# Kernel optimization log

Measured on AMD Instinct MI355X. Metric: run time of the kernel, lower is better.

## Reference

```python
import jax, jax.numpy as jnp
import numpy as np
from jax import lax

B, IN_N, MID_N, OUT_N, K, L, WH = 16, 256, 256, 256, 3, 4096, 1024
EPS = 1e-5


def att_conv(x, W, b=None):
    # x: [B, Cin, L], W: [B, Cout, Cin, K] -> per-sample conv1d, padding='same'
    pl, pr = (K - 1) // 2, K // 2
    xp = jnp.pad(x, ((0, 0), (0, 0), (pl, pr)))
    out = 0.
    for t in range(K):  # small fixed K, unrolled shifted-slice einsum
        out = out + jnp.einsum('bcl,boc->bol', lax.dynamic_slice_in_dim(xp, t, L, 2), W[..., t])
    if b is not None:
        out = out + b[:, :, None]
    return out


def batch_norm(x, w, b):
    # training-mode BN over (N, L) per channel, biased variance
    mean = x.mean((0, 2), keepdims=True)
    var = ((x - mean) ** 2).mean((0, 2), keepdims=True)
    return (x - mean) * (w[None, :, None] / jnp.sqrt(var + EPS)) + b[None, :, None]


def se_module(x, w1, b1, w2, b2):
    s = x.mean(2, keepdims=True)  # [B, C, 1]
    s = jax.nn.relu(jnp.einsum('bcl,oc->bol', s, w1) + b1[None, :, None])
    s = jax.nn.sigmoid(jnp.einsum('bcl,oc->bol', s, w2) + b2[None, :, None])
    return x * s


def setup_inputs() -> dict:
    key = jax.random.key(0)
    ks = jax.random.split(key, 16)
    f = lambda k, sh, sc=0.02: jax.random.normal(k, sh, jnp.float32) * sc
    return {
        'x': f(ks[0], (B, IN_N, L), 1.0),
        'att1': f(ks[1], (B, MID_N, WH), 1.0),
        'att2': f(ks[2], (B, MID_N, WH), 1.0),
        'att3': f(ks[3], (B, OUT_N, WH), 1.0),
        'w1_w': f(ks[4], (IN_N * K, WH)), 'w1_b': jnp.zeros((IN_N * K,), jnp.float32),
        'w2_w': f(ks[5], (MID_N * K, WH)), 'w2_b': jnp.zeros((MID_N * K,), jnp.float32),
        'w3_w': f(ks[6], (MID_N * K, WH)), 'w3_b': jnp.zeros((MID_N * K,), jnp.float32),
        'b1_w': f(ks[7], (1, WH)), 'b1_b': jnp.zeros((1,), jnp.float32),
        'bn2_w': jnp.full((MID_N,), 0.1, jnp.float32), 'bn2_b': jnp.zeros((MID_N,), jnp.float32),
        'bn3_w': jnp.full((OUT_N,), 0.1, jnp.float32), 'bn3_b': jnp.zeros((OUT_N,), jnp.float32),
        'se1_w': f(ks[8], (OUT_N, OUT_N)), 'se1_b': jnp.zeros((OUT_N,), jnp.float32),
        'se2_w': f(ks[9], (OUT_N, OUT_N)), 'se2_b': jnp.zeros((OUT_N,), jnp.float32),
    }


def reference(x, att1, att2, att3, w1_w, w1_b, w2_w, w2_b, w3_w, w3_b,
              b1_w, b1_b, bn2_w, bn2_b, bn3_w, bn3_b, se1_w, se1_b, se2_w, se2_b):
    shortcut = x  # in_n == out_n, no downsample -> Identity
    # hypernetwork weight generation (Linear on last dim)
    W1 = (att1 @ w1_w.T + w1_b).reshape(B, MID_N, IN_N, K)
    W2 = (att2 @ w2_w.T + w2_b).reshape(B, MID_N, MID_N, K)
    W3 = (att3 @ w3_w.T + w3_b).reshape(B, OUT_N, MID_N, K)
    b1 = (att1 @ b1_w.T + b1_b)[..., 0]  # [B, mid_n]
    h = jax.nn.relu(att_conv(x, W1, b1))
    h = jax.nn.relu(batch_norm(att_conv(h, W2), bn2_w, bn2_b))
    h = jax.nn.relu(batch_norm(att_conv(h, W3), bn3_w, bn3_b))
    out = jax.nn.relu(se_module(h, se1_w, se1_b, se2_w, se2_b) + shortcut)
    return out
```

## Files before the change

### kernel.cpp

```cpp
#include <hip/hip_runtime.h>
#include <hip/hip_bf16.h>

using bf16 = __hip_bfloat16;
typedef __attribute__((ext_vector_type(4))) float f32x4;
typedef __attribute__((ext_vector_type(8))) short short8;
typedef __attribute__((ext_vector_type(2))) unsigned int uint2v;
typedef __attribute__((ext_vector_type(4))) unsigned int uint4v;

#define DEVI static __device__ __forceinline__

DEVI unsigned short f2b(float f){
  unsigned int u = __float_as_uint(f);
  unsigned int r = (u + 0x7fffu + ((u >> 16) & 1u)) >> 16;
  return (unsigned short)r;
}
DEVI float b2f(unsigned short u){
  return __uint_as_float(((unsigned int)u) << 16);
}

DEVI void gload16(const void* g, void* l){
  __builtin_amdgcn_global_load_lds(
      (const __attribute__((address_space(1))) unsigned int*)g,
      (__attribute__((address_space(3))) unsigned int*)l, 16, 0, 0);
}

__global__ __launch_bounds__(256) void k_transpose_x(const float* __restrict__ x,
                                                     bf16* __restrict__ xt)
{
  __shared__ float tile[64][65];
  const int b = blockIdx.z, l0 = blockIdx.x*64, c0 = blockIdx.y*64;
  const int tid = threadIdx.x;
  {
    const int r = tid >> 2, q = tid & 3;
    const float* src = x + ((size_t)(b*256 + c0 + r))*4096 + l0 + q*16;
    #pragma unroll
    for (int j = 0; j < 4; ++j){
      const f32x4 v = *reinterpret_cast<const f32x4*>(src + j*4);
      #pragma unroll
      for (int e = 0; e < 4; ++e) tile[r][q*16 + j*4 + e] = v[e];
    }
  }
  __syncthreads();
  {
    const int jr = tid >> 2, cq = tid & 3;
    unsigned int w[8];
    #pragma unroll
    for (int e = 0; e < 8; ++e){
      const float lo = tile[cq*16 + 2*e][jr];
      const float hi = tile[cq*16 + 2*e + 1][jr];
      w[e] = (unsigned int)f2b(lo) | ((unsigned int)f2b(hi) << 16);
    }
    unsigned short* dst = (unsigned short*)xt + ((size_t)b*4098 + l0 + jr + 1)*256 + c0 + cq*16;
    uint4v a0 = {w[0],w[1],w[2],w[3]}, a1 = {w[4],w[5],w[6],w[7]};
    *reinterpret_cast<uint4v*>(dst)     = a0;
    *reinterpret_cast<uint4v*>(dst + 8) = a1;
  }
}

__global__ void k_zero_pads(bf16* __restrict__ xt, bf16* __restrict__ h1t)
{
  const int b = blockIdx.x, tid = threadIdx.x;
  const size_t top = (size_t)b*4098*256 + tid;
  const size_t bot = (size_t)b*4098*256 + (size_t)4097*256 + tid;
  unsigned short* px = (unsigned short*)xt;
  unsigned short* ph = (unsigned short*)h1t;
  px[top] = 0; px[bot] = 0; ph[top] = 0; ph[bot] = 0;
}

__global__ __launch_bounds__(256) void k_cvt3(const float* __restrict__ s0, const float* __restrict__ s1,
                                              const float* __restrict__ s2, bf16* __restrict__ dst, int n1)
{
  const size_t total = (size_t)3 * (size_t)n1 / 4;
  for (size_t i = (size_t)blockIdx.x*256 + threadIdx.x; i < total; i += (size_t)gridDim.x*256){
    const size_t e = i*4;
    const int which = (int)(e / (size_t)n1);
    const size_t off = e - (size_t)which*(size_t)n1;
    const float* s = which==0 ? s0 : which==1 ? s1 : s2;
    const f32x4 v = *reinterpret_cast<const f32x4*>(s + off);
    uint2v p;
    p[0] = (unsigned)f2b(v[0]) | ((unsigned)f2b(v[1])<<16);
    p[1] = (unsigned)f2b(v[2]) | ((unsigned)f2b(v[3])<<16);
    *reinterpret_cast<uint2v*>((unsigned short*)dst + e) = p;
  }
}

__global__ __launch_bounds__(256, 3) void k_gen(const float* __restrict__ att1f, const float* __restrict__ att2f,
                                                const float* __restrict__ att3f, const bf16* __restrict__ wbp,
                                                const float* __restrict__ bias0, const float* __restrict__ bias1,
                                                const float* __restrict__ bias2, bf16* __restrict__ Wt)
{
  __shared__ bf16 sAll[24576];
  const int flat = blockIdx.x + blockIdx.z*64;
  const int xcd = flat & 7, s = flat >> 3;
  const int t = s % 3, u = s / 3;
  const int ch = u & 1;
  const int tau = (u >> 1)*8 + xcd;
  const int i = tau >> 5, boc = tau & 31;
  const int bo0 = boc*128, c0 = ch*128;
  const bf16*  __restrict__ A  = wbp + (size_t)i*768*1024 + (size_t)(c0*3 + t)*1024;
  const float* __restrict__ Bf = ((i==0) ? att1f : (i==1) ? att2f : att3f) + (size_t)bo0*1024;
  const float* __restrict__ bias = (i==0) ? bias0 : (i==1) ? bias1 : bias2;
  const int tid = threadIdx.x, lane = tid & 63, wid = tid >> 6;
  const int wr = wid >> 1, wc = wid & 1;
  const int frow = lane & 15, g = lane >> 4;
  f32x4 acc[4][4] = {};

#define GEN_STAGE(kt, bufi) { \
    _Pragma("unroll") \
    for (int j = 0; j < 2; ++j){ \
      const int q = tid + j*256, r = q >> 2, s3 = q & 3; \
      const int cc = (s3 ^ ((r >> 1) & 3)) * 8; \
      gload16(A + (size_t)r*3072 + (kt)*32 + cc, (char*)sAll + (bufi)*8192 + q*16); \
    } \
    _Pragma("unroll") \
    for (int j = 0; j < 4; ++j){ \
      const int q = tid + j*256, r = q >> 3, s7 = q & 7; \
      const int ss = s7 ^ (r & 7); \
      gload16(Bf + (size_t)r*1024 + (kt)*32 + ss*4, (char*)sAll + 16384 + (bufi)*16384 + q*16); \
    } \
  }

  GEN_STAGE(0, 0);
  #pragma unroll 1
  for (int kt = 0; kt < 32; ++kt){
    const int p = kt & 1;
    if (kt + 1 < 32){
      GEN_STAGE(kt+1, p^1);
      asm volatile("s_waitcnt vmcnt(6)" ::: "memory");
    } else {
      asm volatile("s_waitcnt vmcnt(0)" ::: "memory");
    }
    __builtin_amdgcn_s_barrier();
    const char* pA = (const char*)sAll + p*8192;
    const char* pB = (const char*)sAll + 16384 + p*16384;
    short8 bfr[4];
    #pragma unroll
    for (int n = 0; n < 4; ++n){
      const int row = wc*64 + n*16 + frow;
      const f32x4 f0 = *reinterpret_cast<const f32x4*>(pB + row*128 + (((2*g)  ^ (row & 7))*16));
      const f32x4 f1 = *reinterpret_cast<const f32x4*>(pB + row*128 + (((2*g+1)^ (row & 7))*16));
      unsigned int w0, w1, w2, w3;
      asm("v_cvt_pk_bf16_f32 %0, %1, %2" : "=v"(w0) : "v"(f0[0]), "v"(f0[1]));
      asm("v_cvt_pk_bf16_f32 %0, %1, %2" : "=v"(w1) : "v"(f0[2]), "v"(f0[3]));
      asm("v_cvt_pk_bf16_f32 %0, %1, %2" : "=v"(w2) : "v"(f1[0]), "v"(f1[1]));
      asm("v_cvt_pk_bf16_f32 %0, %1, %2" : "=v"(w3) : "v"(f1[2]), "v"(f1[3]));
      union { uint4v u; short8 sv; } cvtu;
      cvtu.u[0] = w0; cvtu.u[1] = w1; cvtu.u[2] = w2; cvtu.u[3] = w3;
      bfr[n] = cvtu.sv;
    }
    __builtin_amdgcn_s_setprio(1);
    #pragma unroll
    for (int m = 0; m < 4; ++m){
      const int row = wr*64 + m*16 + frow;
      const int sl = g ^ ((row >> 1) & 3);
      const short8 af = *reinterpret_cast<const short8*>(pA + row*64 + sl*16);
      #pragma unroll
      for (int n = 0; n < 4; ++n)
        acc[m][n] = __builtin_amdgcn_mfma_f32_16x16x32_bf16(af, bfr[n], acc[m][n], 0, 0, 0);
    }
    __builtin_amdgcn_s_setprio(0);
    __builtin_amdgcn_s_barrier();
  }
#undef GEN_STAGE

  #pragma unroll
  for (int m = 0; m < 4; ++m){
    const int lcol = wr*64 + m*16 + g*4;
    float bi[4];
    #pragma unroll
    for (int j = 0; j < 4; ++j) bi[j] = bias[(c0 + lcol + j)*3 + t];
    #pragma unroll
    for (int n = 0; n < 4; ++n){
      const int row = wc*64 + n*16 + frow;
      uint2v pk;
      pk[0] = (unsigned)f2b(acc[m][n][0] + bi[0]) | ((unsigned)f2b(acc[m][n][1] + bi[1]) << 16);
      pk[1] = (unsigned)f2b(acc[m][n][2] + bi[2]) | ((unsigned)f2b(acc[m][n][3] + bi[3]) << 16);
      const int chunk = (lcol >> 3) ^ (row & 15);
      *reinterpret_cast<uint2v*>((char*)sAll + row*256 + chunk*16 + (g&1)*8) = pk;
    }
  }
  __syncthreads();
  {
    const int bb = boc >> 1, o0 = (boc & 1)*128;
    char* gp = (char*)Wt + 2*(((((size_t)(i*16 + bb)*3 + t)*256 + o0)*256) + c0);
    #pragma unroll
    for (int it = 0; it < 8; ++it){
      const int row = it*16 + (tid >> 4);
      const int c = tid & 15;
      const int cs2 = c ^ (row & 15);
      const uint4v v = *reinterpret_cast<const uint4v*>((const char*)sAll + row*256 + cs2*16);
      *reinterpret_cast<uint4v*>(gp + (size_t)row*512 + c*16) = v;
    }
  }
}

__global__ __launch_bounds__(256) void k_b1(const float* __restrict__ att1, const float* __restrict__ b1w,
                                            const float* __restrict__ b1b, float* __restrict__ out)
{
  const int m = blockIdx.x*4 + (threadIdx.x >> 6);
  const int lane = threadIdx.x & 63;
  const float* a = att1 + (size_t)m*1024;
  float s = 0.f;
  for (int k = lane*4; k < 1024; k += 256){
    const f32x4 v = *reinterpret_cast<const f32x4*>(a + k);
    const f32x4 w = *reinterpret_cast<const f32x4*>(b1w + k);
    s += v[0]*w[0] + v[1]*w[1] + v[2]*w[2] + v[3]*w[3];
  }
  #pragma unroll
  for (int d = 32; d > 0; d >>= 1) s += __shfl_down(s, d);
  if (lane == 0) out[m] = s + b1b[0];
}

__global__ __launch_bounds__(256, 2) void k_conv(const bf16* __restrict__ Xt, const bf16* __restrict__ W,
                                                 const float* __restrict__ bias, bf16* __restrict__ out,
                                                 int outBatchStride, int outRowOff, int applyRelu,
                                                 float* __restrict__ statSum, float* __restrict__ statSq)
{
  __shared__ char sAll[67584];
  const int flat = blockIdx.x + (blockIdx.z << 6);
  const int xcd = flat & 7, s = flat >> 3;
  const int b = 2*xcd + (s >> 6);
  const int rem = s & 63;
  const int oh = rem >> 5;
  const int l0 = (rem & 31) * 128;
  const int tid = threadIdx.x, lane = tid & 63, wid = tid >> 6;
  const int wr = wid >> 1, wc = wid & 1;
  const int frow = lane & 15, g = lane >> 4;
  f32x4 acc[4][4] = {};

#define CONV_STAGE(ct, bufi) { \
    const bf16* Ab = W + (((size_t)b*3)*256 + oh*128)*256 + (ct)*32; \
    _Pragma("unroll") \
    for (int t = 0; t < 3; ++t){ \
      _Pragma("unroll") \
      for (int j = 0; j < 2; ++j){ \
        const int q = tid + j*256, r = q >> 2; \
        const int cc = ((q & 3) ^ ((r >> 1) & 3)) * 8; \
        gload16(Ab + (size_t)t*65536 + (size_t)r*256 + cc, \
                sAll + (bufi)*24576 + t*8192 + q*16); \
      } \
    } \
    const bf16* Bb = Xt + ((size_t)b*4098 + l0)*256 + (ct)*32; \
    _Pragma("unroll") \
    for (int j = 0; j < 2; ++j){ \
      const int q = tid + j*256, r = q >> 2; \
      const int cc = ((q & 3) ^ ((r >> 1) & 3)) * 8; \
      gload16(Bb + (size_t)r*256 + cc, sAll + 49152 + (bufi)*9216 + q*16); \
    } \
    {  \
      const int q = 512 + (tid & 63), r = q >> 2; \
      const int cc = ((q & 3) ^ ((r >> 1) & 3)) * 8; \
      gload16(Bb + (size_t)r*256 + cc, sAll + 49152 + (bufi)*9216 + q*16); \
    } \
  }

  CONV_STAGE(0, 0);
  #pragma unroll 1
  for (int ct = 0; ct < 8; ++ct){
    const int buf = ct & 1;
    if (ct + 1 < 8){
      CONV_STAGE(ct+1, buf^1);
      asm volatile("s_waitcnt vmcnt(9)" ::: "memory");
    } else {
      asm volatile("s_waitcnt vmcnt(0)" ::: "memory");
    }
    __builtin_amdgcn_s_barrier();
    const char* pA = sAll + buf*24576;
    const char* pB = sAll + 49152 + buf*9216;
    short8 afr[3][4], bfr[3][4];
    #pragma unroll
    for (int t = 0; t < 3; ++t){
      #pragma unroll
      for (int m = 0; m < 4; ++m){
        const int row = wr*64 + m*16 + frow;
        const int sl = g ^ ((row >> 1) & 3);
        afr[t][m] = *reinterpret_cast<const short8*>(pA + t*8192 + row*64 + sl*16);
      }
      #pragma unroll
      for (int n = 0; n < 4; ++n){
        const int rl = wc*64 + n*16 + frow + t;
        const int sl = g ^ ((rl >> 1) & 3);
        bfr[t][n] = *reinterpret_cast<const short8*>(pB + rl*64 + sl*16);
      }
    }
    __builtin_amdgcn_s_setprio(1);
    #pragma unroll
    for (int t = 0; t < 3; ++t)
      #pragma unroll
      for (int m = 0; m < 4; ++m)
        #pragma unroll
        for (int n = 0; n < 4; ++n)
          acc[m][n] = __builtin_amdgcn_mfma_f32_16x16x32_bf16(afr[t][m], bfr[t][n], acc[m][n], 0, 0, 0);
    __builtin_amdgcn_s_setprio(0);
    __builtin_amdgcn_s_barrier();
  }
#undef CONV_STAGE

  float cs[4][4] = {{0.f}}, cq[4][4] = {{0.f}};
  #pragma unroll
  for (int m = 0; m < 4; ++m){
    const int ol = wr*64 + m*16 + g*4;
    float bi[4] = {0.f, 0.f, 0.f, 0.f};
    if (bias){
      const f32x4 bv = *reinterpret_cast<const f32x4*>(bias + b*256 + oh*128 + ol);
      bi[0]=bv[0]; bi[1]=bv[1]; bi[2]=bv[2]; bi[3]=bv[3];
    }
    #pragma unroll
    for (int n = 0; n < 4; ++n){
      const int row = wc*64 + n*16 + frow;
      float v[4];
      #pragma unroll
      for (int j = 0; j < 4; ++j){
        v[j] = acc[m][n][j] + bi[j];
        if (applyRelu) v[j] = fmaxf(v[j], 0.f);
        cs[m][j] += v[j];
        cq[m][j] += v[j]*v[j];
      }
      uint2v pk;
      pk[0] = (unsigned)f2b(v[0]) | ((unsigned)f2b(v[1]) << 16);
      pk[1] = (unsigned)f2b(v[2]) | ((unsigned)f2b(v[3]) << 16);
      const int chunk = (ol >> 3) ^ (row & 15);
      *reinterpret_cast<uint2v*>(sAll + row*256 + chunk*16 + (g&1)*8) = pk;
    }
  }
  __syncthreads();
  {
    char* gp = (char*)out + 2*((size_t)b*outBatchStride + (size_t)(l0 + outRowOff)*256 + oh*128);
    #pragma unroll
    for (int it = 0; it < 8; ++it){
      const int row = it*16 + (tid >> 4);
      const int c = tid & 15;
      const int cs2 = c ^ (row & 15);
      const uint4v v = *reinterpret_cast<const uint4v*>((const char*)sAll + row*256 + cs2*16);
      *reinterpret_cast<uint4v*>(gp + (size_t)row*512 + c*16) = v;
    }
  }
  if (statSum){
    #pragma unroll
    for (int m = 0; m < 4; ++m)
      #pragma unroll
      for (int j = 0; j < 4; ++j){
        #pragma unroll
        for (int d = 1; d < 16; d <<= 1){
          cs[m][j] += __shfl_xor(cs[m][j], d);
          cq[m][j] += __shfl_xor(cq[m][j], d);
        }
      }
    __syncthreads();
    float* ls = (float*)sAll;
    float* lq = ls + 256;
    if (frow == 0){
      #pragma unroll
      for (int m = 0; m < 4; ++m)
        #pragma unroll
        for (int j = 0; j < 4; ++j){
          ls[wid*64 + m*16 + g*4 + j] = cs[m][j];
          lq[wid*64 + m*16 + g*4 + j] = cq[m][j];
        }
    }
    __syncthreads();
    if (tid < 128){
      const int ol = tid, wrI = ol >> 6, idx = ol & 63;
      const float sv = ls[(wrI*2 + 0)*64 + idx] + ls[(wrI*2 + 1)*64 + idx];
      const float qv = lq[(wrI*2 + 0)*64 + idx] + lq[(wrI*2 + 1)*64 + idx];
      atomicAdd(statSum + oh*128 + ol, sv);
      atomicAdd(statSq  + oh*128 + ol, qv);
    }
  }
}

__global__ void k_bnfin(const float* __restrict__ sum, const float* __restrict__ sq,
                        const float* __restrict__ g, const float* __restrict__ bb,
                        float* __restrict__ scale, float* __restrict__ shift)
{
  const int o = threadIdx.x;
  const float inv = 1.f/65536.f;
  const float m = sum[o]*inv;
  const float v = fmaxf(sq[o]*inv - m*m, 0.f);
  const float sc = g[o] / sqrtf(v + 1e-5f);
  scale[o] = sc;
  shift[o] = bb[o] - m*sc;
}

__global__ __launch_bounds__(256) void k_norm2(const bf16* __restrict__ y, const float* __restrict__ scale,
                                               const float* __restrict__ shift, bf16* __restrict__ h)
{
  const int gr = blockIdx.x*8 + (threadIdx.x >> 5);
  const int oc = threadIdx.x & 31;
  const int b = gr / 4098, lp = gr - b*4098;
  unsigned short* dst = (unsigned short*)h + (size_t)gr*256 + oc*8;
  if (lp == 0 || lp == 4097){
    uint4v z = {0u,0u,0u,0u};
    *reinterpret_cast<uint4v*>(dst) = z;
    return;
  }
  const unsigned short* src = (const unsigned short*)y + ((size_t)b*4096 + (lp-1))*256 + oc*8;
  const uint4v in = *reinterpret_cast<const uint4v*>(src);
  const f32x4 sA0 = *reinterpret_cast<const f32x4*>(scale + oc*8);
  const f32x4 sA1 = *reinterpret_cast<const f32x4*>(scale + oc*8 + 4);
  const f32x4 hA0 = *reinterpret_cast<const f32x4*>(shift + oc*8);
  const f32x4 hA1 = *reinterpret_cast<const f32x4*>(shift + oc*8 + 4);
  uint4v ov;
  #pragma unroll
  for (int e = 0; e < 4; ++e){
    const unsigned int w = in[e];
    const float sc0 = (e<2) ? sA0[2*e] : sA1[2*e-4];
    const float sc1 = (e<2) ? sA0[2*e+1] : sA1[2*e-3];
    const float sh0 = (e<2) ? hA0[2*e] : hA1[2*e-4];
    const float sh1 = (e<2) ? hA0[2*e+1] : hA1[2*e-3];
    const float v0 = fmaxf(b2f((unsigned short)(w & 0xffffu))*sc0 + sh0, 0.f);
    const float v1 = fmaxf(b2f((unsigned short)(w >> 16))*sc1 + sh1, 0.f);
    ov[e] = (unsigned)f2b(v0) | ((unsigned)f2b(v1) << 16);
  }
  *reinterpret_cast<uint4v*>(dst) = ov;
}

__global__ __launch_bounds__(256) void k_sum3(const bf16* __restrict__ y, const float* __restrict__ scale,
                                              const float* __restrict__ shift, float* __restrict__ s_sum)
{
  __shared__ float red[8][256];
  const int tid = threadIdx.x;
  const int rr = tid >> 5, oc = tid & 31;
  const size_t row = (size_t)blockIdx.x*8 + rr;
  const int b = (int)(row >> 12);
  const unsigned short* p = (const unsigned short*)y + row*256 + oc*8;
  const uint4v in = *reinterpret_cast<const uint4v*>(p);
  const f32x4 sA0 = *reinterpret_cast<const f32x4*>(scale + oc*8);
  const f32x4 sA1 = *reinterpret_cast<const f32x4*>(scale + oc*8 + 4);
  const f32x4 hA0 = *reinterpret_cast<const f32x4*>(shift + oc*8);
  const f32x4 hA1 = *reinterpret_cast<const f32x4*>(shift + oc*8 + 4);
  float loc[8];
  #pragma unroll
  for (int e = 0; e < 4; ++e){
    const unsigned int w = in[e];
    const float sc0 = (e<2) ? sA0[2*e] : sA1[2*e-4];
    const float sc1 = (e<2) ? sA0[2*e+1] : sA1[2*e-3];
    const float sh0 = (e<2) ? hA0[2*e] : hA1[2*e-4];
    const float sh1 = (e<2) ? hA0[2*e+1] : hA1[2*e-3];
    loc[2*e]   = fmaxf(b2f((unsigned short)(w & 0xffffu))*sc0 + sh0, 0.f);
    loc[2*e+1] = fmaxf(b2f((unsigned short)(w >> 16))*sc1 + sh1, 0.f);
  }
  #pragma unroll
  for (int j = 0; j < 8; ++j) red[rr][oc*8 + j] = loc[j];
  __syncthreads();
  const int o = tid;
  float tot = 0.f;
  #pragma unroll
  for (int r2 = 0; r2 < 8; ++r2) tot += red[r2][o];
  atomicAdd(&s_sum[(size_t)b*256 + o], tot);
}

__global__ __launch_bounds__(256) void k_se(const float* __restrict__ s_sum, const float* __restrict__ w1,
                                            const float* __restrict__ b1, const float* __restrict__ w2,
                                            const float* __restrict__ b2, float* __restrict__ s2)
{
  __shared__ float sv[256];
  __shared__ float t1[256];
  const int b = blockIdx.x, o = threadIdx.x;
  sv[o] = s_sum[(size_t)b*256 + o] * (1.f/4096.f);
  __syncthreads();
  float a = b1[o];
  for (int c = 0; c < 256; ++c) a += w1[(size_t)o*256 + c] * sv[c];
  t1[o] = fmaxf(a, 0.f);
  __syncthreads();
  float a2 = b2[o];
  for (int c = 0; c < 256; ++c) a2 += w2[(size_t)o*256 + c] * t1[c];
  s2[(size_t)b*256 + o] = 1.f / (1.f + expf(-a2));
}

__global__ __launch_bounds__(256) void k_final(const bf16* __restrict__ y3, const bf16* __restrict__ xt,
                                               const float* __restrict__ scale, const float* __restrict__ shift,
                                               const float* __restrict__ s2, float* __restrict__ out)
{
  __shared__ float tH[64][65];
  __shared__ float tX[64][65];
  const int b = blockIdx.z, o0 = blockIdx.y*64, l0 = blockIdx.x*64;
  const int tid = threadIdx.x;
  {
    const int r = tid >> 2, q = tid & 3;
    const int cb = o0 + q*16;
    const unsigned short* sy = (const unsigned short*)y3 + ((size_t)b*4096 + l0 + r)*256 + cb;
    const unsigned short* sx = (const unsigned short*)xt + ((size_t)b*4098 + l0 + r + 1)*256 + cb;
    const uint4v y0 = *reinterpret_cast<const uint4v*>(sy);
    const uint4v y1 = *reinterpret_cast<const uint4v*>(sy + 8);
    const uint4v x0 = *reinterpret_cast<const uint4v*>(sx);
    const uint4v x1 = *reinterpret_cast<const uint4v*>(sx + 8);
    const f32x4 sc0 = *reinterpret_cast<const f32x4*>(scale + cb);
    const f32x4 sc1 = *reinterpret_cast<const f32x4*>(scale + cb + 4);
    const f32x4 sc2 = *reinterpret_cast<const f32x4*>(scale + cb + 8);
    const f32x4 sc3 = *reinterpret_cast<const f32x4*>(scale + cb + 12);
    const f32x4 sh0 = *reinterpret_cast<const f32x4*>(shift + cb);
    const f32x4 sh1 = *reinterpret_cast<const f32x4*>(shift + cb + 4);
    const f32x4 sh2 = *reinterpret_cast<const f32x4*>(shift + cb + 8);
    const f32x4 sh3 = *reinterpret_cast<const f32x4*>(shift + cb + 12);
    #pragma unroll
    for (int e = 0; e < 4; ++e){
      const float a0 = (e<2) ? sc0[2*e] : sc1[2*e-4];
      const float a1 = (e<2) ? sc0[2*e+1] : sc1[2*e-3];
      const float b0 = (e<2) ? sh0[2*e] : sh1[2*e-4];
      const float b1v = (e<2) ? sh0[2*e+1] : sh1[2*e-3];
      tH[r][q*16 + 2*e]     = fmaxf(b2f((unsigned short)(y0[e] & 0xffffu))*a0 + b0, 0.f);
      tH[r][q*16 + 2*e + 1] = fmaxf(b2f((unsigned short)(y0[e] >> 16))*a1 + b1v, 0.f);
      tX[r][q*16 + 2*e]     = b2f((unsigned short)(x0[e] & 0xffffu));
      tX[r][q*16 + 2*e + 1] = b2f((unsigned short)(x0[e] >> 16));
      const float c0v = (e<2) ? sc2[2*e] : sc3[2*e-4];
      const float c1v = (e<2) ? sc2[2*e+1] : sc3[2*e-3];
      const float d0 = (e<2) ? sh2[2*e] : sh3[2*e-4];
      const float d1 = (e<2) ? sh2[2*e+1] : sh3[2*e-3];
      tH[r][q*16 + 8 + 2*e]     = fmaxf(b2f((unsigned short)(y1[e] & 0xffffu))*c0v + d0, 0.f);
      tH[r][q*16 + 8 + 2*e + 1] = fmaxf(b2f((unsigned short)(y1[e] >> 16))*c1v + d1, 0.f);
      tX[r][q*16 + 8 + 2*e]     = b2f((unsigned short)(x1[e] & 0xffffu));
      tX[r][q*16 + 8 + 2*e + 1] = b2f((unsigned short)(x1[e] >> 16));
    }
  }
  __syncthreads();
  {
    const int orow = tid >> 2, q = tid & 3;
    const int o = o0 + orow;
    const float sfac = s2[(size_t)b*256 + o];
    float* dst = out + ((size_t)b*256 + o)*4096 + l0 + q*16;
    #pragma unroll
    for (int k = 0; k < 16; k += 4){
      f32x4 r;
      #pragma unroll
      for (int e = 0; e < 4; ++e)
        r[e] = fmaxf(tH[q*16 + k + e][orow]*sfac + tX[q*16 + k + e][orow], 0.f);
      *reinterpret_cast<f32x4*>(dst + k) = r;
    }
  }
}

extern "C" void kernel_launch(void* const* d_in, const int* in_sizes, int n_in,
                              void* d_out, int out_size, void* d_ws, size_t ws_size,
                              hipStream_t stream)
{
  const float* x     = (const float*)d_in[0];
  const float* att1  = (const float*)d_in[1];
  const float* att2  = (const float*)d_in[2];
  const float* att3  = (const float*)d_in[3];
  const float* w1_w  = (const float*)d_in[4];
  const float* w1_b  = (const float*)d_in[5];
  const float* w2_w  = (const float*)d_in[6];
  const float* w2_b  = (const float*)d_in[7];
  const float* w3_w  = (const float*)d_in[8];
  const float* w3_b  = (const float*)d_in[9];
  const float* b1_w  = (const float*)d_in[10];
  const float* b1_b  = (const float*)d_in[11];
  const float* bn2_w = (const float*)d_in[12];
  const float* bn2_b = (const float*)d_in[13];
  const float* bn3_w = (const float*)d_in[14];
  const float* bn3_b = (const float*)d_in[15];
  const float* se1_w = (const float*)d_in[16];
  const float* se1_b = (const float*)d_in[17];
  const float* se2_w = (const float*)d_in[18];
  const float* se2_b = (const float*)d_in[19];

  char* ws = (char*)d_ws;
  bf16*  xT   = (bf16*)(ws + 0);
  bf16*  h1T  = (bf16*)(ws + 33570816);
  bf16*  y2T  = (bf16*)(ws + 67141632);
  bf16*  h2T  = (bf16*)(ws + 100696064);
  bf16*  Wt   = (bf16*)(ws + 134266880);
  bf16*  wb   = (bf16*)(ws + 178307072);
  float* b1v  = (float*)(ws + 183025664);
  float* st   = (float*)(ws + 183042048);
  float* bn2sum = st;
  float* bn2sq  = st + 256;
  float* bn3sum = st + 512;
  float* bn3sq  = st + 768;
  float* s_sum  = st + 1024;
  float* scale2 = st + 5120;
  float* shift2 = st + 5376;
  float* scale3 = st + 5632;
  float* shift3 = st + 5888;
  float* s2v    = st + 6144;
  bf16*  y3T  = (bf16*)(ws + 33570816);

  hipMemsetAsync(st, 0, 5120*sizeof(float), stream);

  k_transpose_x<<<dim3(64,4,16),256,0,stream>>>(x, xT);
  k_zero_pads<<<16,256,0,stream>>>(xT, h1T);
  k_cvt3<<<512,256,0,stream>>>(w1_w, w2_w, w3_w, wb, 768*1024);
  k_gen<<<dim3(64,1,9),256,0,stream>>>(att1, att2, att3, wb, w1_b, w2_b, w3_b, Wt);
  k_b1<<<1024,256,0,stream>>>(att1, b1_w, b1_b, b1v);

  k_conv<<<dim3(64,1,16),256,0,stream>>>(xT,  Wt,                           b1v,     h1T, 4098*256, 1, 1, nullptr, nullptr);
  k_conv<<<dim3(64,1,16),256,0,stream>>>(h1T, Wt + (size_t)1*16*3*256*256,  nullptr, y2T, 4096*256, 0, 0, bn2sum, bn2sq);
  k_bnfin<<<1,256,0,stream>>>(bn2sum, bn2sq, bn2_w, bn2_b, scale2, shift2);
  k_norm2<<<8196,256,0,stream>>>(y2T, scale2, shift2, h2T);
  k_conv<<<dim3(64,1,16),256,0,stream>>>(h2T, Wt + (size_t)2*16*3*256*256,  nullptr, y3T, 4096*256, 0, 0, bn3sum, bn3sq);
  k_bnfin<<<1,256,0,stream>>>(bn3sum, bn3sq, bn3_w, bn3_b, scale3, shift3);
  k_sum3<<<8192,256,0,stream>>>(y3T, scale3, shift3, s_sum);
  k_se<<<16,256,0,stream>>>(s_sum, se1_w, se1_b, se2_w, se2_b, s2v);
  k_final<<<dim3(64,4,16),256,0,stream>>>(y3T, xT, scale3, shift3, s2v, (float*)d_out);
}
```

Baseline: 297.6 us.

## Convert hypernetwork fp32 attention tiles to bf16 once before staging into LDS

In the weight-generation GEMM kernel, the fp32 attention operand is no longer copied straight into LDS by global-to-LDS loads. It is now loaded into registers, converted to bf16 once per thread, and written into a swizzled bf16 LDS buffer after the MFMA phase of the previous step. This halves the LDS footprint of the B tile and removes the repeated per-wave fp32 loads and conversions at fragment-read time. In exchange, the loads go through registers and the LDS write lands after the compute phase, which adds register pressure and an extra LDS wait before each barrier.

```diff
diff --git a/kernel.cpp b/kernel.cpp
--- a/kernel.cpp
+++ b/kernel.cpp
@@ -89,7 +89,7 @@
                                                 const float* __restrict__ bias0, const float* __restrict__ bias1,
                                                 const float* __restrict__ bias2, bf16* __restrict__ Wt)
 {
-  __shared__ bf16 sAll[24576];
+  __shared__ bf16 sAll[16384];
   const int flat = blockIdx.x + blockIdx.z*64;
   const int xcd = flat & 7, s = flat >> 3;
   const int t = s % 3, u = s / 3;
@@ -104,49 +104,64 @@
   const int wr = wid >> 1, wc = wid & 1;
   const int frow = lane & 15, g = lane >> 4;
   f32x4 acc[4][4] = {};
-
-#define GEN_STAGE(kt, bufi) { \
+  f32x4 rB[4];
+
+  const int rowB = tid >> 1, hB = tid & 1;
+  const float* bsBase = Bf + (size_t)rowB*1024 + hB*16;
+  const int swB = (rowB >> 1) & 3;
+  const int cB0 = (2*hB)     ^ swB;
+  const int cB1 = (2*hB + 1) ^ swB;
+
+#define GEN_STAGE(kt) { \
+    _Pragma("unroll") \
+    for (int q4 = 0; q4 < 4; ++q4) rB[q4] = *reinterpret_cast<const f32x4*>(bsBase + (kt)*32 + q4*4); \
     _Pragma("unroll") \
     for (int j = 0; j < 2; ++j){ \
       const int q = tid + j*256, r = q >> 2, s3 = q & 3; \
       const int cc = (s3 ^ ((r >> 1) & 3)) * 8; \
-      gload16(A + (size_t)r*3072 + (kt)*32 + cc, (char*)sAll + (bufi)*8192 + q*16); \
-    } \
-    _Pragma("unroll") \
-    for (int j = 0; j < 4; ++j){ \
-      const int q = tid + j*256, r = q >> 3, s7 = q & 7; \
-      const int ss = s7 ^ (r & 7); \
-      gload16(Bf + (size_t)r*1024 + (kt)*32 + ss*4, (char*)sAll + 16384 + (bufi)*16384 + q*16); \
-    } \
-  }
-
-  GEN_STAGE(0, 0);
+      gload16(A + (size_t)r*3072 + (kt)*32 + cc, (char*)sAll + (((kt)&1)*8192) + q*16); \
+    } }
+
+#define GEN_WRITEB(kt) { \
+    unsigned int w0, w1, w2, w3; \
+    asm("v_cvt_pk_bf16_f32 %0, %1, %2" : "=v"(w0) : "v"(rB[0][0]), "v"(rB[0][1])); \
+    asm("v_cvt_pk_bf16_f32 %0, %1, %2" : "=v"(w1) : "v"(rB[0][2]), "v"(rB[0][3])); \
+    asm("v_cvt_pk_bf16_f32 %0, %1, %2" : "=v"(w2) : "v"(rB[1][0]), "v"(rB[1][1])); \
+    asm("v_cvt_pk_bf16_f32 %0, %1, %2" : "=v"(w3) : "v"(rB[1][2]), "v"(rB[1][3])); \
+    uint4v pk0; pk0[0]=w0; pk0[1]=w1; pk0[2]=w2; pk0[3]=w3; \
+    asm("v_cvt_pk_bf16_f32 %0, %1, %2" : "=v"(w0) : "v"(rB[2][0]), "v"(rB[2][1])); \
+    asm("v_cvt_pk_bf16_f32 %0, %1, %2" : "=v"(w1) : "v"(rB[2][2]), "v"(rB[2][3])); \
+    asm("v_cvt_pk_bf16_f32 %0, %1, %2" : "=v"(w2) : "v"(rB[3][0]), "v"(rB[3][1])); \
+    asm("v_cvt_pk_bf16_f32 %0, %1, %2" : "=v"(w3) : "v"(rB[3][2]), "v"(rB[3][3])); \
+    uint4v pk1; pk1[0]=w0; pk1[1]=w1; pk1[2]=w2; pk1[3]=w3; \
+    char* wb_ = (char*)sAll + 16384 + (((kt)&1)*8192) + rowB*64; \
+    *reinterpret_cast<uint4v*>(wb_ + cB0*16) = pk0; \
+    *reinterpret_cast<uint4v*>(wb_ + cB1*16) = pk1; }
+
+  GEN_STAGE(0);
+  asm volatile("s_waitcnt vmcnt(0)" ::: "memory");
+  GEN_WRITEB(0);
+  asm volatile("s_waitcnt lgkmcnt(0)" ::: "memory");
+  __builtin_amdgcn_s_barrier();
+
   #pragma unroll 1
   for (int kt = 0; kt < 32; ++kt){
     const int p = kt & 1;
     if (kt + 1 < 32){
-      GEN_STAGE(kt+1, p^1);
+      GEN_STAGE(kt+1);
       asm volatile("s_waitcnt vmcnt(6)" ::: "memory");
     } else {
       asm volatile("s_waitcnt vmcnt(0)" ::: "memory");
     }
     __builtin_amdgcn_s_barrier();
     const char* pA = (const char*)sAll + p*8192;
-    const char* pB = (const char*)sAll + 16384 + p*16384;
+    const char* pB = (const char*)sAll + 16384 + p*8192;
     short8 bfr[4];
     #pragma unroll
     for (int n = 0; n < 4; ++n){
       const int row = wc*64 + n*16 + frow;
-      const f32x4 f0 = *reinterpret_cast<const f32x4*>(pB + row*128 + (((2*g)  ^ (row & 7))*16));
-      const f32x4 f1 = *reinterpret_cast<const f32x4*>(pB + row*128 + (((2*g+1)^ (row & 7))*16));
-      unsigned int w0, w1, w2, w3;
-      asm("v_cvt_pk_bf16_f32 %0, %1, %2" : "=v"(w0) : "v"(f0[0]), "v"(f0[1]));
-      asm("v_cvt_pk_bf16_f32 %0, %1, %2" : "=v"(w1) : "v"(f0[2]), "v"(f0[3]));
-      asm("v_cvt_pk_bf16_f32 %0, %1, %2" : "=v"(w2) : "v"(f1[0]), "v"(f1[1]));
-      asm("v_cvt_pk_bf16_f32 %0, %1, %2" : "=v"(w3) : "v"(f1[2]), "v"(f1[3]));
-      union { uint4v u; short8 sv; } cvtu;
-      cvtu.u[0] = w0; cvtu.u[1] = w1; cvtu.u[2] = w2; cvtu.u[3] = w3;
-      bfr[n] = cvtu.sv;
+      const int sl = g ^ ((row >> 1) & 3);
+      bfr[n] = *reinterpret_cast<const short8*>(pB + row*64 + sl*16);
     }
     __builtin_amdgcn_s_setprio(1);
     #pragma unroll
@@ -159,9 +174,14 @@
         acc[m][n] = __builtin_amdgcn_mfma_f32_16x16x32_bf16(af, bfr[n], acc[m][n], 0, 0, 0);
     }
     __builtin_amdgcn_s_setprio(0);
+    if (kt + 1 < 32){
+      GEN_WRITEB(kt+1);
+    }
+    asm volatile("s_waitcnt lgkmcnt(0)" ::: "memory");
     __builtin_amdgcn_s_barrier();
   }
 #undef GEN_STAGE
+#undef GEN_WRITEB
 
   #pragma unroll
   for (int m = 0; m < 4; ++m){
```

Result: slower. 313.4 us (+5.3%).

## Merge transpose, pad-zero, weight-gen and b1 kernels into one front launch

Applied to the files above, without the earlier changes.

Combines four independent preprocessing kernels (x transpose, pad zeroing, hypernetwork weight generation GEMM, and b1 dot products) into a single kernel that dispatches on block index ranges. The intent is to cut launch overhead and let the memory-bound transpose and b1 blocks run alongside the compute-bound gen GEMM blocks. The cost is that every block now reserves the larger 48KB shared allocation and the launch-bounds register budget of the GEMM path, which may limit occupancy for the lightweight block types.

```diff
diff --git a/kernel.cpp b/kernel.cpp
--- a/kernel.cpp
+++ b/kernel.cpp
@@ -22,49 +22,6 @@
   __builtin_amdgcn_global_load_lds(
       (const __attribute__((address_space(1))) unsigned int*)g,
       (__attribute__((address_space(3))) unsigned int*)l, 16, 0, 0);
-}
-
-__global__ __launch_bounds__(256) void k_transpose_x(const float* __restrict__ x,
-                                                     bf16* __restrict__ xt)
-{
-  __shared__ float tile[64][65];
-  const int b = blockIdx.z, l0 = blockIdx.x*64, c0 = blockIdx.y*64;
-  const int tid = threadIdx.x;
-  {
-    const int r = tid >> 2, q = tid & 3;
-    const float* src = x + ((size_t)(b*256 + c0 + r))*4096 + l0 + q*16;
-    #pragma unroll
-    for (int j = 0; j < 4; ++j){
-      const f32x4 v = *reinterpret_cast<const f32x4*>(src + j*4);
-      #pragma unroll
-      for (int e = 0; e < 4; ++e) tile[r][q*16 + j*4 + e] = v[e];
-    }
-  }
-  __syncthreads();
-  {
-    const int jr = tid >> 2, cq = tid & 3;
-    unsigned int w[8];
-    #pragma unroll
-    for (int e = 0; e < 8; ++e){
-      const float lo = tile[cq*16 + 2*e][jr];
-      const float hi = tile[cq*16 + 2*e + 1][jr];
-      w[e] = (unsigned int)f2b(lo) | ((unsigned int)f2b(hi) << 16);
-    }
-    unsigned short* dst = (unsigned short*)xt + ((size_t)b*4098 + l0 + jr + 1)*256 + c0 + cq*16;
-    uint4v a0 = {w[0],w[1],w[2],w[3]}, a1 = {w[4],w[5],w[6],w[7]};
-    *reinterpret_cast<uint4v*>(dst)     = a0;
-    *reinterpret_cast<uint4v*>(dst + 8) = a1;
-  }
-}
-
-__global__ void k_zero_pads(bf16* __restrict__ xt, bf16* __restrict__ h1t)
-{
-  const int b = blockIdx.x, tid = threadIdx.x;
-  const size_t top = (size_t)b*4098*256 + tid;
-  const size_t bot = (size_t)b*4098*256 + (size_t)4097*256 + tid;
-  unsigned short* px = (unsigned short*)xt;
-  unsigned short* ph = (unsigned short*)h1t;
-  px[top] = 0; px[bot] = 0; ph[top] = 0; ph[bot] = 0;
 }
 
 __global__ __launch_bounds__(256) void k_cvt3(const float* __restrict__ s0, const float* __restrict__ s1,
@@ -84,26 +41,35 @@
   }
 }
 
-__global__ __launch_bounds__(256, 3) void k_gen(const float* __restrict__ att1f, const float* __restrict__ att2f,
-                                                const float* __restrict__ att3f, const bf16* __restrict__ wbp,
-                                                const float* __restrict__ bias0, const float* __restrict__ bias1,
-                                                const float* __restrict__ bias2, bf16* __restrict__ Wt)
-{
-  __shared__ bf16 sAll[24576];
-  const int flat = blockIdx.x + blockIdx.z*64;
-  const int xcd = flat & 7, s = flat >> 3;
-  const int t = s % 3, u = s / 3;
-  const int ch = u & 1;
-  const int tau = (u >> 1)*8 + xcd;
-  const int i = tau >> 5, boc = tau & 31;
-  const int bo0 = boc*128, c0 = ch*128;
-  const bf16*  __restrict__ A  = wbp + (size_t)i*768*1024 + (size_t)(c0*3 + t)*1024;
-  const float* __restrict__ Bf = ((i==0) ? att1f : (i==1) ? att2f : att3f) + (size_t)bo0*1024;
-  const float* __restrict__ bias = (i==0) ? bias0 : (i==1) ? bias1 : bias2;
-  const int tid = threadIdx.x, lane = tid & 63, wid = tid >> 6;
-  const int wr = wid >> 1, wc = wid & 1;
-  const int frow = lane & 15, g = lane >> 4;
-  f32x4 acc[4][4] = {};
+__global__ __launch_bounds__(256, 3) void k_front(
+    const float* __restrict__ x, bf16* __restrict__ xt, bf16* __restrict__ h1t,
+    const float* __restrict__ att1f, const float* __restrict__ att2f,
+    const float* __restrict__ att3f, const bf16* __restrict__ wbp,
+    const float* __restrict__ bias0, const float* __restrict__ bias1,
+    const float* __restrict__ bias2, bf16* __restrict__ Wt,
+    const float* __restrict__ b1w, const float* __restrict__ b1b,
+    float* __restrict__ b1out)
+{
+  __shared__ char sMem[49152];
+  const int bid = blockIdx.x;
+  const int tid = threadIdx.x;
+
+  if (bid < 576){
+    bf16* sAll = (bf16*)sMem;
+    const int flat = bid;
+    const int xcd = flat & 7, s = flat >> 3;
+    const int t = s % 3, u = s / 3;
+    const int ch = u & 1;
+    const int tau = (u >> 1)*8 + xcd;
+    const int i = tau >> 5, boc = tau & 31;
+    const int bo0 = boc*128, c0 = ch*128;
+    const bf16*  __restrict__ A  = wbp + (size_t)i*768*1024 + (size_t)(c0*3 + t)*1024;
+    const float* __restrict__ Bf = ((i==0) ? att1f : (i==1) ? att2f : att3f) + (size_t)bo0*1024;
+    const float* __restrict__ bias = (i==0) ? bias0 : (i==1) ? bias1 : bias2;
+    const int lane = tid & 63, wid = tid >> 6;
+    const int wr = wid >> 1, wc = wid & 1;
+    const int frow = lane & 15, g = lane >> 4;
+    f32x4 acc[4][4] = {};
 
 #define GEN_STAGE(kt, bufi) { \
     _Pragma("unroll") \
@@ -120,95 +86,140 @@
     } \
   }
 
-  GEN_STAGE(0, 0);
-  #pragma unroll 1
-  for (int kt = 0; kt < 32; ++kt){
-    const int p = kt & 1;
-    if (kt + 1 < 32){
-      GEN_STAGE(kt+1, p^1);
-      asm volatile("s_waitcnt vmcnt(6)" ::: "memory");
-    } else {
-      asm volatile("s_waitcnt vmcnt(0)" ::: "memory");
-    }
-    __builtin_amdgcn_s_barrier();
-    const char* pA = (const char*)sAll + p*8192;
-    const char* pB = (const char*)sAll + 16384 + p*16384;
-    short8 bfr[4];
-    #pragma unroll
-    for (int n = 0; n < 4; ++n){
-      const int row = wc*64 + n*16 + frow;
-      const f32x4 f0 = *reinterpret_cast<const f32x4*>(pB + row*128 + (((2*g)  ^ (row & 7))*16));
-      const f32x4 f1 = *reinterpret_cast<const f32x4*>(pB + row*128 + (((2*g+1)^ (row & 7))*16));
-      unsigned int w0, w1, w2, w3;
-      asm("v_cvt_pk_bf16_f32 %0, %1, %2" : "=v"(w0) : "v"(f0[0]), "v"(f0[1]));
-      asm("v_cvt_pk_bf16_f32 %0, %1, %2" : "=v"(w1) : "v"(f0[2]), "v"(f0[3]));
-      asm("v_cvt_pk_bf16_f32 %0, %1, %2" : "=v"(w2) : "v"(f1[0]), "v"(f1[1]));
-      asm("v_cvt_pk_bf16_f32 %0, %1, %2" : "=v"(w3) : "v"(f1[2]), "v"(f1[3]));
-      union { uint4v u; short8 sv; } cvtu;
-      cvtu.u[0] = w0; cvtu.u[1] = w1; cvtu.u[2] = w2; cvtu.u[3] = w3;
-      bfr[n] = cvtu.sv;
-    }
-    __builtin_amdgcn_s_setprio(1);
+    GEN_STAGE(0, 0);
+    #pragma unroll 1
+    for (int kt = 0; kt < 32; ++kt){
+      const int p = kt & 1;
+      if (kt + 1 < 32){
+        GEN_STAGE(kt+1, p^1);
+        asm volatile("s_waitcnt vmcnt(6)" ::: "memory");
+      } else {
+        asm volatile("s_waitcnt vmcnt(0)" ::: "memory");
+      }
+      __builtin_amdgcn_s_barrier();
+      const char* pA = (const char*)sAll + p*8192;
+      const char* pB = (const char*)sAll + 16384 + p*16384;
+      short8 bfr[4];
+      #pragma unroll
+      for (int n = 0; n < 4; ++n){
+        const int row = wc*64 + n*16 + frow;
+        const f32x4 f0 = *reinterpret_cast<const f32x4*>(pB + row*128 + (((2*g)  ^ (row & 7))*16));
+        const f32x4 f1 = *reinterpret_cast<const f32x4*>(pB + row*128 + (((2*g+1)^ (row & 7))*16));
+        unsigned int w0, w1, w2, w3;
+        asm("v_cvt_pk_bf16_f32 %0, %1, %2" : "=v"(w0) : "v"(f0[0]), "v"(f0[1]));
+        asm("v_cvt_pk_bf16_f32 %0, %1, %2" : "=v"(w1) : "v"(f0[2]), "v"(f0[3]));
+        asm("v_cvt_pk_bf16_f32 %0, %1, %2" : "=v"(w2) : "v"(f1[0]), "v"(f1[1]));
+        asm("v_cvt_pk_bf16_f32 %0, %1, %2" : "=v"(w3) : "v"(f1[2]), "v"(f1[3]));
+        union { uint4v u4; short8 sv; } cvtu;
+        cvtu.u4[0] = w0; cvtu.u4[1] = w1; cvtu.u4[2] = w2; cvtu.u4[3] = w3;
+        bfr[n] = cvtu.sv;
+      }
+      __builtin_amdgcn_s_setprio(1);
+      #pragma unroll
+      for (int m = 0; m < 4; ++m){
+        const int row = wr*64 + m*16 + frow;
+        const int sl = g ^ ((row >> 1) & 3);
+        const short8 af = *reinterpret_cast<const short8*>(pA + row*64 + sl*16);
+        #pragma unroll
+        for (int n = 0; n < 4; ++n)
+          acc[m][n] = __builtin_amdgcn_mfma_f32_16x16x32_bf16(af, bfr[n], acc[m][n], 0, 0, 0);
+      }
+      __builtin_amdgcn_s_setprio(0);
+      __builtin_amdgcn_s_barrier();
+    }
+#undef GEN_STAGE
+
     #pragma unroll
     for (int m = 0; m < 4; ++m){
-      const int row = wr*64 + m*16 + frow;
-      const int sl = g ^ ((row >> 1) & 3);
-      const short8 af = *reinterpret_cast<const short8*>(pA + row*64 + sl*16);
-      #pragma unroll
-      for (int n = 0; n < 4; ++n)
-        acc[m][n] = __builtin_amdgcn_mfma_f32_16x16x32_bf16(af, bfr[n], acc[m][n], 0, 0, 0);
-    }
-    __builtin_amdgcn_s_setprio(0);
-    __builtin_amdgcn_s_barrier();
-  }
-#undef GEN_STAGE
-
-  #pragma unroll
-  for (int m = 0; m < 4; ++m){
-    const int lcol = wr*64 + m*16 + g*4;
-    float bi[4];
-    #pragma unroll
-    for (int j = 0; j < 4; ++j) bi[j] = bias[(c0 + lcol + j)*3 + t];
-    #pragma unroll
-    for (int n = 0; n < 4; ++n){
-      const int row = wc*64 + n*16 + frow;
-      uint2v pk;
-      pk[0] = (unsigned)f2b(acc[m][n][0] + bi[0]) | ((unsigned)f2b(acc[m][n][1] + bi[1]) << 16);
-      pk[1] = (unsigned)f2b(acc[m][n][2] + bi[2]) | ((unsigned)f2b(acc[m][n][3] + bi[3]) << 16);
-      const int chunk = (lcol >> 3) ^ (row & 15);
-      *reinterpret_cast<uint2v*>((char*)sAll + row*256 + chunk*16 + (g&1)*8) = pk;
-    }
-  }
-  __syncthreads();
+      const int lcol = wr*64 + m*16 + g*4;
+      float bi[4];
+      #pragma unroll
+      for (int j = 0; j < 4; ++j) bi[j] = bias[(c0 + lcol + j)*3 + t];
+      #pragma unroll
+      for (int n = 0; n < 4; ++n){
+        const int row = wc*64 + n*16 + frow;
+        uint2v pk;
+        pk[0] = (unsigned)f2b(acc[m][n][0] + bi[0]) | ((unsigned)f2b(acc[m][n][1] + bi[1]) << 16);
+        pk[1] = (unsigned)f2b(acc[m][n][2] + bi[2]) | ((unsigned)f2b(acc[m][n][3] + bi[3]) << 16);
+        const int chunk = (lcol >> 3) ^ (row & 15);
+        *reinterpret_cast<uint2v*>((char*)sAll + row*256 + chunk*16 + (g&1)*8) = pk;
+      }
+    }
+    __syncthreads();
+    {
+      const int bb = boc >> 1, o0 = (boc & 1)*128;
+      char* gp = (char*)Wt + 2*(((((size_t)(i*16 + bb)*3 + t)*256 + o0)*256) + c0);
+      #pragma unroll
+      for (int it = 0; it < 8; ++it){
+        const int row = it*16 + (tid >> 4);
+        const int c = tid & 15;
+        const int cs2 = c ^ (row & 15);
+        const uint4v v = *reinterpret_cast<const uint4v*>((const char*)sAll + row*256 + cs2*16);
+        *reinterpret_cast<uint4v*>(gp + (size_t)row*512 + c*16) = v;
+      }
+    }
+    return;
+  }
+
+  if (bid < 4672){
+    float (*tile)[65] = reinterpret_cast<float(*)[65]>(sMem);
+    const int r2 = bid - 576;
+    const int b = r2 >> 8;
+    const int rem = r2 & 255;
+    const int c0 = ((rem >> 6) & 3)*64;
+    const int l0 = (rem & 63)*64;
+    {
+      const int r = tid >> 2, q = tid & 3;
+      const float* src = x + ((size_t)(b*256 + c0 + r))*4096 + l0 + q*16;
+      #pragma unroll
+      for (int j = 0; j < 4; ++j){
+        const f32x4 v = *reinterpret_cast<const f32x4*>(src + j*4);
+        #pragma unroll
+        for (int e = 0; e < 4; ++e) tile[r][q*16 + j*4 + e] = v[e];
+      }
+    }
+    __syncthreads();
+    {
+      const int jr = tid >> 2, cq = tid & 3;
+      unsigned int w[8];
+      #pragma unroll
+      for (int e = 0; e < 8; ++e){
+        const float lo = tile[cq*16 + 2*e][jr];
+        const float hi = tile[cq*16 + 2*e + 1][jr];
+        w[e] = (unsigned int)f2b(lo) | ((unsigned int)f2b(hi) << 16);
+      }
+      unsigned short* dst = (unsigned short*)xt + ((size_t)b*4098 + l0 + jr + 1)*256 + c0 + cq*16;
+      uint4v a0 = {w[0],w[1],w[2],w[3]}, a1 = {w[4],w[5],w[6],w[7]};
+      *reinterpret_cast<uint4v*>(dst)     = a0;
+      *reinterpret_cast<uint4v*>(dst + 8) = a1;
+    }
+    return;
+  }
+
+  if (bid < 4688){
+    const int b = bid - 4672;
+    const size_t top = (size_t)b*4098*256 + tid;
+    const size_t bot = (size_t)b*4098*256 + (size_t)4097*256 + tid;
+    unsigned short* px = (unsigned short*)xt;
+    unsigned short* ph = (unsigned short*)h1t;
+    px[top] = 0; px[bot] = 0; ph[top] = 0; ph[bot] = 0;
+    return;
+  }
+
   {
-    const int bb = boc >> 1, o0 = (boc & 1)*128;
-    char* gp = (char*)Wt + 2*(((((size_t)(i*16 + bb)*3 + t)*256 + o0)*256) + c0);
-    #pragma unroll
-    for (int it = 0; it < 8; ++it){
-      const int row = it*16 + (tid >> 4);
-      const int c = tid & 15;
-      const int cs2 = c ^ (row & 15);
-      const uint4v v = *reinterpret_cast<const uint4v*>((const char*)sAll + row*256 + cs2*16);
-      *reinterpret_cast<uint4v*>(gp + (size_t)row*512 + c*16) = v;
-    }
-  }
-}
-
-__global__ __launch_bounds__(256) void k_b1(const float* __restrict__ att1, const float* __restrict__ b1w,
-                                            const float* __restrict__ b1b, float* __restrict__ out)
-{
-  const int m = blockIdx.x*4 + (threadIdx.x >> 6);
-  const int lane = threadIdx.x & 63;
-  const float* a = att1 + (size_t)m*1024;
-  float s = 0.f;
-  for (int k = lane*4; k < 1024; k += 256){
-    const f32x4 v = *reinterpret_cast<const f32x4*>(a + k);
-    const f32x4 w = *reinterpret_cast<const f32x4*>(b1w + k);
-    s += v[0]*w[0] + v[1]*w[1] + v[2]*w[2] + v[3]*w[3];
-  }
-  #pragma unroll
-  for (int d = 32; d > 0; d >>= 1) s += __shfl_down(s, d);
-  if (lane == 0) out[m] = s + b1b[0];
+    const int m = (bid - 4688)*4 + (tid >> 6);
+    const int lane = tid & 63;
+    const float* a = att1f + (size_t)m*1024;
+    float s = 0.f;
+    for (int k = lane*4; k < 1024; k += 256){
+      const f32x4 v = *reinterpret_cast<const f32x4*>(a + k);
+      const f32x4 w = *reinterpret_cast<const f32x4*>(b1w + k);
+      s += v[0]*w[0] + v[1]*w[1] + v[2]*w[2] + v[3]*w[3];
+    }
+    #pragma unroll
+    for (int d = 32; d > 0; d >>= 1) s += __shfl_down(s, d);
+    if (lane == 0) b1out[m] = s + b1b[0];
+  }
 }
 
 __global__ __launch_bounds__(256, 2) void k_conv(const bf16* __restrict__ Xt, const bf16* __restrict__ W,
@@ -578,11 +589,9 @@
 
   hipMemsetAsync(st, 0, 5120*sizeof(float), stream);
 
-  k_transpose_x<<<dim3(64,4,16),256,0,stream>>>(x, xT);
-  k_zero_pads<<<16,256,0,stream>>>(xT, h1T);
   k_cvt3<<<512,256,0,stream>>>(w1_w, w2_w, w3_w, wb, 768*1024);
-  k_gen<<<dim3(64,1,9),256,0,stream>>>(att1, att2, att3, wb, w1_b, w2_b, w3_b, Wt);
-  k_b1<<<1024,256,0,stream>>>(att1, b1_w, b1_b, b1v);
+  k_front<<<5712,256,0,stream>>>(x, xT, h1T, att1, att2, att3, wb,
+                                 w1_b, w2_b, w3_b, Wt, b1_w, b1_b, b1v);
 
   k_conv<<<dim3(64,1,16),256,0,stream>>>(xT,  Wt,                           b1v,     h1T, 4098*256, 1, 1, nullptr, nullptr);
   k_conv<<<dim3(64,1,16),256,0,stream>>>(h1T, Wt + (size_t)1*16*3*256*256,  nullptr, y2T, 4096*256, 0, 0, bn2sum, bn2sq);
```

New measurement: 284.4 us. -4.4%, faster.
